# Optimization experiments

Hardware: AMD Instinct MI355X
Metric: run time of the kernel (lower is better)

Reference implementation:

```python
import jax, jax.numpy as jnp
import numpy as np
from itertools import product

B, D, H, W_, C = 2, 64, 64, 64, 96
OUT = 192  # c_multiplier * dim
EPS = 1e-5


def setup_inputs() -> dict:
    key = jax.random.key(0)
    k1, k2 = jax.random.split(key)
    x = jax.random.normal(k1, (B, D, H, W_, C), dtype=jnp.float32)
    ln_w = jnp.ones((8 * C,), dtype=jnp.float32)
    ln_b = jnp.zeros((8 * C,), dtype=jnp.float32)
    W = jax.random.normal(k2, (OUT, 8 * C), dtype=jnp.float32) * 0.02
    return {"x": x, "ln_w": ln_w, "ln_b": ln_b, "W": W}


def reference(x, ln_w, ln_b, W):
    # strided patch gather + concat: order matches itertools.product over (0,1)^3
    parts = [x[:, s0::2, s1::2, s2::2, :] for s0, s1, s2 in product((0, 1), repeat=3)]
    y = jnp.concatenate(parts, axis=-1)  # [B, D/2, H/2, W/2, 8C]
    # LayerNorm over last dim
    mu = jnp.mean(y, axis=-1, keepdims=True)
    var = jnp.mean(jnp.square(y - mu), axis=-1, keepdims=True)
    y = (y - mu) * jax.lax.rsqrt(var + EPS) * ln_w + ln_b
    # linear reduction (bias=False); torch Linear weight is [out, in]
    return jnp.einsum('bdhwc,oc->bdhwo', y, W)
```

## Files before the change

### kernel.cpp

```cpp
#include <hip/hip_runtime.h>
#include <stdint.h>

#define C_IN   96
#define KIN    768
#define NOUT   192
#define MTILE  32
#define LDK    772
#define EPS    1e-5f
#define NKIT   24

typedef __bf16 bf16x8 __attribute__((ext_vector_type(8)));
typedef float  f32x4  __attribute__((ext_vector_type(4)));

static __device__ __forceinline__ unsigned int f2bf(float f) {
    union { float f; unsigned int u; } v; v.f = f;
    return (v.u + 0x7fffu + ((v.u >> 16) & 1u)) >> 16;
}
static __device__ __forceinline__ float bf2f(unsigned int s) {
    union { unsigned int u; float f; } v; v.u = s << 16;
    return v.f;
}

__global__ __launch_bounds__(256) void prep_bias(
    const float* __restrict__ W, const float* __restrict__ lnw,
    const float* __restrict__ lnb, float* __restrict__ bias,
    float* __restrict__ Scol)
{
    int o = blockIdx.x;
    int tid = threadIdx.x;
    float bpart = 0.f, spart = 0.f;
    for (int c = tid; c < KIN; c += 256) {
        float w = W[(size_t)o * KIN + c];
        spart += bf2f(f2bf(w * lnw[c]));
        bpart += w * lnb[c];
    }
    #pragma unroll
    for (int m = 32; m >= 1; m >>= 1) {
        bpart += __shfl_xor(bpart, m, 64);
        spart += __shfl_xor(spart, m, 64);
    }
    __shared__ float redb[4], reds[4];
    if ((tid & 63) == 0) { redb[tid >> 6] = bpart; reds[tid >> 6] = spart; }
    __syncthreads();
    if (tid == 0) {
        bias[o] = redb[0] + redb[1] + redb[2] + redb[3];
        Scol[o] = reds[0] + reds[1] + reds[2] + reds[3];
    }
}

__global__ __launch_bounds__(256) void prep_swz(
    const float* __restrict__ W, const float* __restrict__ lnw,
    unsigned short* __restrict__ Wsw)
{
    const int nt = blockIdx.x;
    for (int s = threadIdx.x; s < NKIT * 64; s += 256) {
        const int kk = s >> 6;
        const int l  = s & 63;
        const int row = nt * 16 + (l & 15);
        const int k0  = kk * 32 + (l >> 4) * 8;
        const float* src = W + (size_t)row * KIN + k0;
        unsigned int p[4];
        #pragma unroll
        for (int j = 0; j < 4; ++j) {
            float a = src[2 * j]     * lnw[k0 + 2 * j];
            float b = src[2 * j + 1] * lnw[k0 + 2 * j + 1];
            p[j] = f2bf(a) | (f2bf(b) << 16);
        }
        *(uint4*)&Wsw[(size_t)((nt * NKIT + kk) * 64 + l) * 8] =
            make_uint4(p[0], p[1], p[2], p[3]);
    }
}

__global__ __launch_bounds__(256, 3) void merge_kernel(
    const float* __restrict__ x, const unsigned short* __restrict__ Wsw,
    const float* __restrict__ bias, const float* __restrict__ Scol,
    float* __restrict__ out)
{
    __shared__ unsigned short ylds[MTILE * LDK];
    __shared__ float muL[MTILE], rsL[MTILE];

    const int tid   = threadIdx.x;
    const int tbase = blockIdx.x * MTILE;
    const int bh = blockIdx.x;
    const int h  = bh & 31;
    const int d  = (bh >> 5) & 31;
    const int b  = bh >> 10;

    const int tk = tid >> 3;
    const int i  = tid & 7;
    const float* base = x +
        ((size_t)((b * 64 + 2 * d) * 64 + 2 * h) * 64 + 2 * tk) * C_IN + i * 4;

    const int OFF[8] = {0, 96, 6144, 6240, 393216, 393312, 399360, 399456};

    float4 v[24];
    #pragma unroll
    for (int g = 0; g < 8; ++g)
        #pragma unroll
        for (int jj = 0; jj < 3; ++jj)
            v[g * 3 + jj] = *(const float4*)(base + OFF[g] + jj * 32);

    __builtin_amdgcn_sched_barrier(0);

    float sum = 0.f, sq = 0.f;
    #pragma unroll
    for (int g = 0; g < 8; ++g) {
        #pragma unroll
        for (int jj = 0; jj < 3; ++jj) {
            float4 t = v[g * 3 + jj];
            sum += t.x + t.y + t.z + t.w;
            sq  += t.x * t.x + t.y * t.y + t.z * t.z + t.w * t.w;
            uint2 p;
            p.x = f2bf(t.x) | (f2bf(t.y) << 16);
            p.y = f2bf(t.z) | (f2bf(t.w) << 16);
            *(uint2*)&ylds[tk * LDK + g * 96 + (i + jj * 8) * 4] = p;
        }
    }
    #pragma unroll
    for (int m = 4; m >= 1; m >>= 1) {
        sum += __shfl_xor(sum, m, 8);
        sq  += __shfl_xor(sq,  m, 8);
    }
    if (i == 0) {
        float mean = sum * (1.f / 768.f);
        float var  = sq * (1.f / 768.f) - mean * mean;
        muL[tk] = mean;
        rsL[tk] = rsqrtf(var + EPS);
    }
    __syncthreads();

    const int wv    = tid >> 6;
    const int l     = tid & 63;
    const int l15   = l & 15;
    const int quad  = l >> 4;
    const int nbase = wv * 48;
    const int koff  = quad * 8;

    f32x4 acc[2][3];
    #pragma unroll
    for (int mt = 0; mt < 2; ++mt)
        #pragma unroll
        for (int nt = 0; nt < 3; ++nt)
            acc[mt][nt] = (f32x4){0.f, 0.f, 0.f, 0.f};

    const unsigned short* arow0 = &ylds[l15        * LDK + koff];
    const unsigned short* arow1 = &ylds[(16 + l15) * LDK + koff];
    const unsigned short* bp0 = Wsw + ((size_t)((3 * wv + 0) * NKIT) * 64 + l) * 8;
    const unsigned short* bp1 = Wsw + ((size_t)((3 * wv + 1) * NKIT) * 64 + l) * 8;
    const unsigned short* bp2 = Wsw + ((size_t)((3 * wv + 2) * NKIT) * 64 + l) * 8;

    bf16x8 A0[2], A1[2], B0[2], B1[2], B2[2];
    #pragma unroll
    for (int p = 0; p < 2; ++p) {
        A0[p] = *(const bf16x8*)(arow0 + p * 32);
        A1[p] = *(const bf16x8*)(arow1 + p * 32);
        B0[p] = *(const bf16x8*)(bp0 + p * 512);
        B1[p] = *(const bf16x8*)(bp1 + p * 512);
        B2[p] = *(const bf16x8*)(bp2 + p * 512);
    }
    #pragma unroll
    for (int kk = 0; kk < NKIT; ++kk) {
        const int c = kk & 1;
        bf16x8 na0, na1, nb0, nb1, nb2;
        if (kk < NKIT - 2) {
            const int k2 = kk + 2;
            na0 = *(const bf16x8*)(arow0 + k2 * 32);
            na1 = *(const bf16x8*)(arow1 + k2 * 32);
            nb0 = *(const bf16x8*)(bp0 + k2 * 512);
            nb1 = *(const bf16x8*)(bp1 + k2 * 512);
            nb2 = *(const bf16x8*)(bp2 + k2 * 512);
        }
        acc[0][0] = __builtin_amdgcn_mfma_f32_16x16x32_bf16(A0[c], B0[c], acc[0][0], 0, 0, 0);
        acc[0][1] = __builtin_amdgcn_mfma_f32_16x16x32_bf16(A0[c], B1[c], acc[0][1], 0, 0, 0);
        acc[0][2] = __builtin_amdgcn_mfma_f32_16x16x32_bf16(A0[c], B2[c], acc[0][2], 0, 0, 0);
        acc[1][0] = __builtin_amdgcn_mfma_f32_16x16x32_bf16(A1[c], B0[c], acc[1][0], 0, 0, 0);
        acc[1][1] = __builtin_amdgcn_mfma_f32_16x16x32_bf16(A1[c], B1[c], acc[1][1], 0, 0, 0);
        acc[1][2] = __builtin_amdgcn_mfma_f32_16x16x32_bf16(A1[c], B2[c], acc[1][2], 0, 0, 0);
        if (kk < NKIT - 2) {
            A0[c] = na0; A1[c] = na1; B0[c] = nb0; B1[c] = nb1; B2[c] = nb2;
        }
    }

    const float S0 = Scol[nbase + l15];
    const float S1 = Scol[nbase + 16 + l15];
    const float S2 = Scol[nbase + 32 + l15];
    const float c0 = bias[nbase + l15];
    const float c1 = bias[nbase + 16 + l15];
    const float c2 = bias[nbase + 32 + l15];
    #pragma unroll
    for (int mt = 0; mt < 2; ++mt) {
        #pragma unroll
        for (int r = 0; r < 4; ++r) {
            const int row = mt * 16 + quad * 4 + r;
            const float rs = rsL[row];
            const float rm = rs * muL[row];
            float* op = out + (size_t)(tbase + row) * NOUT + nbase + l15;
            op[0]  = rs * acc[mt][0][r] - rm * S0 + c0;
            op[16] = rs * acc[mt][1][r] - rm * S1 + c1;
            op[32] = rs * acc[mt][2][r] - rm * S2 + c2;
        }
    }
}

extern "C" void kernel_launch(void* const* d_in, const int* in_sizes, int n_in,
                              void* d_out, int out_size, void* d_ws, size_t ws_size,
                              hipStream_t stream) {
    const float* x   = (const float*)d_in[0];
    const float* lnw = (const float*)d_in[1];
    const float* lnb = (const float*)d_in[2];
    const float* W   = (const float*)d_in[3];
    float* out = (float*)d_out;

    unsigned short* Wsw = (unsigned short*)d_ws;
    float* bias = (float*)((char*)d_ws + (size_t)NOUT * KIN * 2);
    float* Scol = bias + NOUT;

    prep_bias<<<NOUT, 256, 0, stream>>>(W, lnw, lnb, bias, Scol);
    prep_swz<<<12, 256, 0, stream>>>(W, lnw, Wsw);
    merge_kernel<<<2048, 256, 0, stream>>>(x, Wsw, bias, Scol, out);
}
```

Baseline: 324.1 us.

## Split fused merge into repack-to-bf16 pass and a separate MFMA GEMM kernel

Replaces the single fused gather+LayerNorm+GEMM kernel with two kernels. A repack kernel gathers the strided patches, converts them to bf16 in an MFMA-fragment layout (with an XOR swizzle in LDS) and writes per-token mean/rstd. A GEMM kernel then streams A fragments directly from global memory with larger per-wave tiles (2x6 MFMA tiles). This removes LDS staging and the in-kernel sync from the GEMM, but adds an extra global round trip of the bf16 activations (about 100 MB write plus read) and another kernel launch.

```diff
diff --git a/kernel.cpp b/kernel.cpp
--- a/kernel.cpp
+++ b/kernel.cpp
@@ -4,8 +4,6 @@
 #define C_IN   96
 #define KIN    768
 #define NOUT   192
-#define MTILE  32
-#define LDK    772
 #define EPS    1e-5f
 #define NKIT   24
 
@@ -19,6 +17,9 @@
 static __device__ __forceinline__ float bf2f(unsigned int s) {
     union { unsigned int u; float f; } v; v.u = s << 16;
     return v.f;
+}
+static __device__ __forceinline__ int swz(int a) {
+    return a ^ (((a >> 8) & 7) << 4);
 }
 
 __global__ __launch_bounds__(256) void prep_bias(
@@ -71,133 +72,164 @@
     }
 }
 
-__global__ __launch_bounds__(256, 3) void merge_kernel(
-    const float* __restrict__ x, const unsigned short* __restrict__ Wsw,
+__global__ __launch_bounds__(256) void repack_kernel(
+    const float* __restrict__ x, unsigned short* __restrict__ yt,
+    float2* __restrict__ stats)
+{
+    __shared__ unsigned char tile[24576 + 64];
+
+    const int tid = threadIdx.x;
+    const int mt  = blockIdx.x;
+    const int b  = mt >> 11;
+    const int d  = (mt >> 6) & 31;
+    const int h  = (mt >> 1) & 31;
+    const int wh = mt & 1;
+
+    const int r = tid >> 6;
+    const int l = tid & 63;
+    const int s0 = r >> 1, s1 = r & 1;
+    const float* src = x +
+        (((size_t)(b * 64 + 2 * d + s0) * 64 + (2 * h + s1)) * 64 + wh * 32) * C_IN
+        + l * 4;
+
+    float4 v[12];
+    #pragma unroll
+    for (int it = 0; it < 12; ++it)
+        v[it] = *(const float4*)(src + it * 256);
+    __builtin_amdgcn_sched_barrier(0);
+
+    #pragma unroll
+    for (int it = 0; it < 12; ++it) {
+        const int p  = it * 256 + l * 4;
+        const int t5 = p >> 5;
+        const int xw = (t5 * 171) >> 9;
+        const int c  = p - xw * 96;
+        const int m  = xw >> 1;
+        const int k  = (r * 2 + (xw & 1)) * 96 + c;
+        const int kk = k >> 5, quad = (k >> 3) & 3, sub = (k & 4) << 1;
+        const int addr = ((kk << 6) + m + (quad << 4)) * 16 + sub;
+        uint2 pk;
+        pk.x = f2bf(v[it].x) | (f2bf(v[it].y) << 16);
+        pk.y = f2bf(v[it].z) | (f2bf(v[it].w) << 16);
+        *(uint2*)(tile + swz(addr)) = pk;
+    }
+    __syncthreads();
+
+    char* dst = (char*)yt + (size_t)mt * 24576;
+    #pragma unroll
+    for (int s = 0; s < 6; ++s) {
+        const int lin = s * 4096 + tid * 16;
+        *(uint4*)(dst + lin) = *(const uint4*)(tile + swz(lin));
+    }
+
+    {
+        const int m = tid >> 4, j = tid & 15;
+        float sum = 0.f, sq = 0.f;
+        #pragma unroll
+        for (int e6 = 0; e6 < 6; ++e6) {
+            const int e  = j + e6 * 16;
+            const int kk = e >> 2, quad = e & 3;
+            const int a  = ((kk << 6) + m + (quad << 4)) * 16;
+            uint4 u = *(const uint4*)(tile + swz(a));
+            const unsigned int w[4] = {u.x, u.y, u.z, u.w};
+            #pragma unroll
+            for (int q = 0; q < 4; ++q) {
+                float lo = bf2f(w[q] & 0xffffu);
+                float hi = bf2f(w[q] >> 16);
+                sum += lo + hi;
+                sq  += lo * lo + hi * hi;
+            }
+        }
+        #pragma unroll
+        for (int msk = 1; msk <= 8; msk <<= 1) {
+            sum += __shfl_xor(sum, msk, 16);
+            sq  += __shfl_xor(sq,  msk, 16);
+        }
+        if (j == 0) {
+            float mean = sum * (1.f / 768.f);
+            float var  = sq * (1.f / 768.f) - mean * mean;
+            stats[mt * 16 + m] = make_float2(mean, rsqrtf(var + EPS));
+        }
+    }
+}
+
+__global__ __launch_bounds__(256, 3) void gemm_kernel(
+    const unsigned short* __restrict__ yt, const unsigned short* __restrict__ Wsw,
     const float* __restrict__ bias, const float* __restrict__ Scol,
-    float* __restrict__ out)
-{
-    __shared__ unsigned short ylds[MTILE * LDK];
-    __shared__ float muL[MTILE], rsL[MTILE];
-
-    const int tid   = threadIdx.x;
-    const int tbase = blockIdx.x * MTILE;
-    const int bh = blockIdx.x;
-    const int h  = bh & 31;
-    const int d  = (bh >> 5) & 31;
-    const int b  = bh >> 10;
-
-    const int tk = tid >> 3;
-    const int i  = tid & 7;
-    const float* base = x +
-        ((size_t)((b * 64 + 2 * d) * 64 + 2 * h) * 64 + 2 * tk) * C_IN + i * 4;
-
-    const int OFF[8] = {0, 96, 6144, 6240, 393216, 393312, 399360, 399456};
-
-    float4 v[24];
-    #pragma unroll
-    for (int g = 0; g < 8; ++g)
-        #pragma unroll
-        for (int jj = 0; jj < 3; ++jj)
-            v[g * 3 + jj] = *(const float4*)(base + OFF[g] + jj * 32);
-
-    __builtin_amdgcn_sched_barrier(0);
-
-    float sum = 0.f, sq = 0.f;
-    #pragma unroll
-    for (int g = 0; g < 8; ++g) {
-        #pragma unroll
-        for (int jj = 0; jj < 3; ++jj) {
-            float4 t = v[g * 3 + jj];
-            sum += t.x + t.y + t.z + t.w;
-            sq  += t.x * t.x + t.y * t.y + t.z * t.z + t.w * t.w;
-            uint2 p;
-            p.x = f2bf(t.x) | (f2bf(t.y) << 16);
-            p.y = f2bf(t.z) | (f2bf(t.w) << 16);
-            *(uint2*)&ylds[tk * LDK + g * 96 + (i + jj * 8) * 4] = p;
-        }
-    }
-    #pragma unroll
-    for (int m = 4; m >= 1; m >>= 1) {
-        sum += __shfl_xor(sum, m, 8);
-        sq  += __shfl_xor(sq,  m, 8);
-    }
-    if (i == 0) {
-        float mean = sum * (1.f / 768.f);
-        float var  = sq * (1.f / 768.f) - mean * mean;
-        muL[tk] = mean;
-        rsL[tk] = rsqrtf(var + EPS);
-    }
-    __syncthreads();
-
-    const int wv    = tid >> 6;
-    const int l     = tid & 63;
-    const int l15   = l & 15;
-    const int quad  = l >> 4;
-    const int nbase = wv * 48;
-    const int koff  = quad * 8;
-
-    f32x4 acc[2][3];
-    #pragma unroll
-    for (int mt = 0; mt < 2; ++mt)
-        #pragma unroll
-        for (int nt = 0; nt < 3; ++nt)
-            acc[mt][nt] = (f32x4){0.f, 0.f, 0.f, 0.f};
-
-    const unsigned short* arow0 = &ylds[l15        * LDK + koff];
-    const unsigned short* arow1 = &ylds[(16 + l15) * LDK + koff];
-    const unsigned short* bp0 = Wsw + ((size_t)((3 * wv + 0) * NKIT) * 64 + l) * 8;
-    const unsigned short* bp1 = Wsw + ((size_t)((3 * wv + 1) * NKIT) * 64 + l) * 8;
-    const unsigned short* bp2 = Wsw + ((size_t)((3 * wv + 2) * NKIT) * 64 + l) * 8;
-
-    bf16x8 A0[2], A1[2], B0[2], B1[2], B2[2];
+    const float2* __restrict__ stats, float* __restrict__ out)
+{
+    const int tid  = threadIdx.x;
+    const int wv   = tid >> 6;
+    const int l    = tid & 63;
+    const int l15  = l & 15;
+    const int quad = l >> 4;
+    const int nh   = wv & 1;
+    const int mt0  = blockIdx.x * 4 + (wv >> 1) * 2;
+
+    const char* aptr0 = (const char*)yt + (size_t)mt0 * 24576 + l * 16;
+    const char* aptr1 = aptr0 + 24576;
+    const char* bptr  = (const char*)Wsw + (size_t)nh * 6 * NKIT * 1024 + l * 16;
+
+    f32x4 acc[2][6];
+    #pragma unroll
+    for (int mi = 0; mi < 2; ++mi)
+        #pragma unroll
+        for (int nt = 0; nt < 6; ++nt)
+            acc[mi][nt] = (f32x4){0.f, 0.f, 0.f, 0.f};
+
+    bf16x8 A[2][2], Bv[2][6];
     #pragma unroll
     for (int p = 0; p < 2; ++p) {
-        A0[p] = *(const bf16x8*)(arow0 + p * 32);
-        A1[p] = *(const bf16x8*)(arow1 + p * 32);
-        B0[p] = *(const bf16x8*)(bp0 + p * 512);
-        B1[p] = *(const bf16x8*)(bp1 + p * 512);
-        B2[p] = *(const bf16x8*)(bp2 + p * 512);
+        A[p][0] = *(const bf16x8*)(aptr0 + p * 1024);
+        A[p][1] = *(const bf16x8*)(aptr1 + p * 1024);
+        #pragma unroll
+        for (int nt = 0; nt < 6; ++nt)
+            Bv[p][nt] = *(const bf16x8*)(bptr + (size_t)(nt * NKIT + p) * 1024);
     }
     #pragma unroll
     for (int kk = 0; kk < NKIT; ++kk) {
         const int c = kk & 1;
-        bf16x8 na0, na1, nb0, nb1, nb2;
+        bf16x8 nA0, nA1, nB[6];
         if (kk < NKIT - 2) {
             const int k2 = kk + 2;
-            na0 = *(const bf16x8*)(arow0 + k2 * 32);
-            na1 = *(const bf16x8*)(arow1 + k2 * 32);
-            nb0 = *(const bf16x8*)(bp0 + k2 * 512);
-            nb1 = *(const bf16x8*)(bp1 + k2 * 512);
-            nb2 = *(const bf16x8*)(bp2 + k2 * 512);
-        }
-        acc[0][0] = __builtin_amdgcn_mfma_f32_16x16x32_bf16(A0[c], B0[c], acc[0][0], 0, 0, 0);
-        acc[0][1] = __builtin_amdgcn_mfma_f32_16x16x32_bf16(A0[c], B1[c], acc[0][1], 0, 0, 0);
-        acc[0][2] = __builtin_amdgcn_mfma_f32_16x16x32_bf16(A0[c], B2[c], acc[0][2], 0, 0, 0);
-        acc[1][0] = __builtin_amdgcn_mfma_f32_16x16x32_bf16(A1[c], B0[c], acc[1][0], 0, 0, 0);
-        acc[1][1] = __builtin_amdgcn_mfma_f32_16x16x32_bf16(A1[c], B1[c], acc[1][1], 0, 0, 0);
-        acc[1][2] = __builtin_amdgcn_mfma_f32_16x16x32_bf16(A1[c], B2[c], acc[1][2], 0, 0, 0);
+            nA0 = *(const bf16x8*)(aptr0 + k2 * 1024);
+            nA1 = *(const bf16x8*)(aptr1 + k2 * 1024);
+            #pragma unroll
+            for (int nt = 0; nt < 6; ++nt)
+                nB[nt] = *(const bf16x8*)(bptr + (size_t)(nt * NKIT + k2) * 1024);
+        }
+        #pragma unroll
+        for (int nt = 0; nt < 6; ++nt) {
+            acc[0][nt] = __builtin_amdgcn_mfma_f32_16x16x32_bf16(A[c][0], Bv[c][nt], acc[0][nt], 0, 0, 0);
+            acc[1][nt] = __builtin_amdgcn_mfma_f32_16x16x32_bf16(A[c][1], Bv[c][nt], acc[1][nt], 0, 0, 0);
+        }
         if (kk < NKIT - 2) {
-            A0[c] = na0; A1[c] = na1; B0[c] = nb0; B1[c] = nb1; B2[c] = nb2;
-        }
-    }
-
-    const float S0 = Scol[nbase + l15];
-    const float S1 = Scol[nbase + 16 + l15];
-    const float S2 = Scol[nbase + 32 + l15];
-    const float c0 = bias[nbase + l15];
-    const float c1 = bias[nbase + 16 + l15];
-    const float c2 = bias[nbase + 32 + l15];
-    #pragma unroll
-    for (int mt = 0; mt < 2; ++mt) {
-        #pragma unroll
-        for (int r = 0; r < 4; ++r) {
-            const int row = mt * 16 + quad * 4 + r;
-            const float rs = rsL[row];
-            const float rm = rs * muL[row];
-            float* op = out + (size_t)(tbase + row) * NOUT + nbase + l15;
-            op[0]  = rs * acc[mt][0][r] - rm * S0 + c0;
-            op[16] = rs * acc[mt][1][r] - rm * S1 + c1;
-            op[32] = rs * acc[mt][2][r] - rm * S2 + c2;
+            A[c][0] = nA0; A[c][1] = nA1;
+            #pragma unroll
+            for (int nt = 0; nt < 6; ++nt) Bv[c][nt] = nB[nt];
+        }
+    }
+
+    float2 st[2][4];
+    #pragma unroll
+    for (int mi = 0; mi < 2; ++mi)
+        #pragma unroll
+        for (int rr = 0; rr < 4; ++rr)
+            st[mi][rr] = stats[(mt0 + mi) * 16 + quad * 4 + rr];
+
+    #pragma unroll
+    for (int nt = 0; nt < 6; ++nt) {
+        const int col = nh * 96 + nt * 16 + l15;
+        const float S = Scol[col];
+        const float bc = bias[col];
+        #pragma unroll
+        for (int mi = 0; mi < 2; ++mi) {
+            #pragma unroll
+            for (int rr = 0; rr < 4; ++rr) {
+                const int t = (mt0 + mi) * 16 + quad * 4 + rr;
+                const float mu = st[mi][rr].x, rs = st[mi][rr].y;
+                out[(size_t)t * NOUT + col] = rs * acc[mi][nt][rr] - rs * mu * S + bc;
+            }
         }
     }
 }
@@ -211,11 +243,15 @@
     const float* W   = (const float*)d_in[3];
     float* out = (float*)d_out;
 
-    unsigned short* Wsw = (unsigned short*)d_ws;
-    float* bias = (float*)((char*)d_ws + (size_t)NOUT * KIN * 2);
-    float* Scol = bias + NOUT;
+    char* ws = (char*)d_ws;
+    unsigned short* Wsw  = (unsigned short*)ws;
+    float* bias          = (float*)(ws + 294912);
+    float* Scol          = (float*)(ws + 295680);
+    float2* stats        = (float2*)(ws + 296448);
+    unsigned short* yt   = (unsigned short*)(ws + 1048576);
 
     prep_bias<<<NOUT, 256, 0, stream>>>(W, lnw, lnb, bias, Scol);
     prep_swz<<<12, 256, 0, stream>>>(W, lnw, Wsw);
-    merge_kernel<<<2048, 256, 0, stream>>>(x, Wsw, bias, Scol, out);
-}
+    repack_kernel<<<4096, 256, 0, stream>>>(x, yt, stats);
+    gemm_kernel<<<1024, 256, 0, stream>>>(yt, Wsw, bias, Scol, stats, out);
+}
```

Measured after the change: 399.7 us. 1.23x slower.
